# Performance work log

Measured on AMD Instinct MI355X. Metric: run time of the kernel, lower is better.

The kernel has to match this reference:

```python
import jax, jax.numpy as jnp
import numpy as np

C = 512
HEADS = 8
HEAD_DIM = 64
OUT = 2560
NEG = -1.0e12
EPS = 1e-5


def _layernorm(x, g, b):
    mu = jnp.mean(x, axis=-1, keepdims=True)
    var = jnp.mean(jnp.square(x - mu), axis=-1, keepdims=True)
    return (x - mu) * jax.lax.rsqrt(var + EPS) * g + b


def setup_inputs() -> dict:
    key = jax.random.key(0)
    ks = jax.random.split(key, 16)
    s = 0.02
    return {
        "x": jax.random.normal(ks[0], (8, C, 32, 32), dtype=jnp.float32),
        "conv_w": jax.random.normal(ks[1], (C, C), dtype=jnp.float32) * s,
        "conv_b": jnp.zeros((C,), jnp.float32),
        "ln_g": jnp.ones((C,), jnp.float32),
        "ln_b": jnp.zeros((C,), jnp.float32),
        "qkv_w": jax.random.normal(ks[2], (3 * C, C), dtype=jnp.float32) * s,
        "qkv_b": jnp.zeros((3 * C,), jnp.float32),
        "proj_w": jax.random.normal(ks[3], (C, C), dtype=jnp.float32) * s,
        "proj_b": jnp.zeros((C,), jnp.float32),
        "w1": jax.random.normal(ks[4], (C, C), dtype=jnp.float32) * s,
        "b1": jnp.zeros((C,), jnp.float32),
        "w2": jax.random.normal(ks[5], (C, C), dtype=jnp.float32) * s,
        "b2": jnp.zeros((C,), jnp.float32),
        "fc_w": jax.random.normal(ks[6], (OUT, C), dtype=jnp.float32) * s,
        "fc_b": jnp.zeros((OUT,), jnp.float32),
    }


def reference(x, conv_w, conv_b, ln_g, ln_b, qkv_w, qkv_b, proj_w, proj_b,
              w1, b1, w2, b2, fc_w, fc_b):
    B, Cc, H, W = x.shape
    N = H * W
    mk = jax.random.split(jax.random.key(42), 3)

    # Flat1D: conv1x1 == per-pixel linear, then flatten -> [B, N, C]
    t = jnp.einsum('bchw,oc->bhwo', x, conv_w) + conv_b
    t = t.reshape(B, N, Cc)

    # LayerNorm (shared params)
    t = _layernorm(t, ln_g, ln_b)

    # Attention with random additive mask (p=0.5)
    qkv = t @ qkv_w.T + qkv_b  # [B, N, 3C]
    qkv = qkv.reshape(B, N, 3, HEADS, Cc // HEADS)
    q = jnp.transpose(qkv[:, :, 0], (0, 2, 1, 3))  # [B, H, N, D]
    k = jnp.transpose(qkv[:, :, 1], (0, 2, 1, 3))
    v = jnp.transpose(qkv[:, :, 2], (0, 2, 1, 3))
    scale = HEAD_DIM ** (-0.5)
    attn = jnp.einsum('bhnd,bhmd->bhnm', q, k) * scale
    amask = jax.random.bernoulli(mk[0], 0.5, attn.shape)
    attn = attn + amask.astype(attn.dtype) * NEG
    attn = jax.nn.softmax(attn, axis=-1)
    o = jnp.einsum('bhnm,bhmd->bhnd', attn, v)
    o = jnp.transpose(o, (0, 2, 1, 3)).reshape(B, N, Cc)
    t = o @ proj_w.T + proj_b

    # FeedForward with random additive masks
    h = jax.nn.gelu(t @ w1.T + b1, approximate=False)
    m1 = jax.random.bernoulli(mk[1], 0.3, h.shape)
    h = h + m1.astype(h.dtype) * NEG
    t = h @ w2.T + b2
    m2 = jax.random.bernoulli(mk[2], 0.1, t.shape)
    t = t + m2.astype(t.dtype) * NEG

    # LayerNorm (same params), mean over tokens, final fc
    t = _layernorm(t, ln_g, ln_b)
    t = jnp.mean(t, axis=1)  # [B, C]
    return t @ fc_w.T + fc_b
```

## Files before the change

kernel.cpp:

```cpp
#include <hip/hip_runtime.h>
#include <stdint.h>
#include <math.h>

#define NEGV -1.0e12f
#define QSCALE 0.18033688011112042f

typedef __attribute__((ext_vector_type(8))) short bf16x8;
typedef __attribute__((ext_vector_type(4))) float f32x4;
typedef __attribute__((ext_vector_type(8))) ushort u16x8;

#define ROTL1(v, r) ({ uint32_t _d;                                            \
    asm("v_alignbit_b32 %0, %1, %1, %2" : "=v"(_d) : "v"(v), "n"(32 - (r)));   \
    _d; })

#if defined(__has_builtin)
#if __has_builtin(__builtin_amdgcn_exp2f)
#define EXP2(x) __builtin_amdgcn_exp2f(x)
#endif
#endif
#ifndef EXP2
#define EXP2(x) exp2f(x)
#endif

__host__ static void tf2x32_host(uint32_t k0, uint32_t k1, uint32_t c0, uint32_t c1,
                                 uint32_t* o0, uint32_t* o1) {
    uint32_t ks2 = k0 ^ k1 ^ 0x1BD11BDAu;
    uint32_t x0 = c0 + k0, x1 = c1 + k1;
#define TF_RND(r) x0 += x1; x1 = ((x1 << (r)) | (x1 >> (32 - (r)))); x1 ^= x0;
    TF_RND(13) TF_RND(15) TF_RND(26) TF_RND(6)
    x0 += k1;  x1 += ks2 + 1u;
    TF_RND(17) TF_RND(29) TF_RND(16) TF_RND(24)
    x0 += ks2; x1 += k0 + 2u;
    TF_RND(13) TF_RND(15) TF_RND(26) TF_RND(6)
    x0 += k0;  x1 += k1 + 3u;
    TF_RND(17) TF_RND(29) TF_RND(16) TF_RND(24)
    x0 += k1;  x1 += ks2 + 4u;
    TF_RND(13) TF_RND(15) TF_RND(26) TF_RND(6)
    x0 += ks2; x1 += k0 + 5u;
#undef TF_RND
    *o0 = x0; *o1 = x1;
}

__device__ __forceinline__ uint32_t tf_bits(uint32_t k0, uint32_t k1, uint32_t j) {
    const uint32_t ks2 = k0 ^ k1 ^ 0x1BD11BDAu;
    uint32_t x0 = k0, x1 = j + k1;
#define TFR(r) x0 += x1; x1 = ROTL1(x1, r); x1 ^= x0;
    TFR(13) TFR(15) TFR(26) TFR(6)
    x0 += k1;  x1 += ks2 + 1u;
    TFR(17) TFR(29) TFR(16) TFR(24)
    x0 += ks2; x1 += k0 + 2u;
    TFR(13) TFR(15) TFR(26) TFR(6)
    x0 += k0;  x1 += k1 + 3u;
    TFR(17) TFR(29) TFR(16) TFR(24)
    x0 += k1;  x1 += ks2 + 4u;
    TFR(13) TFR(15) TFR(26) TFR(6)
#undef TFR
    return (x0 + ks2) ^ (x1 + (k0 + 5u));
}

__host__ static uint32_t maskT(float p) {
    double t = ceil((double)p * 8388608.0);
    return ((uint32_t)t) << 9;
}

__device__ __forceinline__ ushort f2bf(float x) {
    uint32_t u = __float_as_uint(x);
    u += 0x7fffu + ((u >> 16) & 1u);
    return (ushort)(u >> 16);
}
__device__ __forceinline__ float bf2f(ushort u) {
    return __uint_as_float(((uint32_t)u) << 16);
}

__global__ __launch_bounds__(256) void prep_k(const float* __restrict__ x,
                                              ushort* __restrict__ xt,
                                              const float* __restrict__ s0,
                                              const float* __restrict__ s1,
                                              const float* __restrict__ s2,
                                              const float* __restrict__ s3,
                                              const float* __restrict__ s4,
                                              ushort* __restrict__ wdst)
{
    __shared__ float tile[64][65];
    const int tid = threadIdx.x;
    if (blockIdx.x < 1024) {
        const int id = blockIdx.x;
        const int n0 = (id & 15) * 64, c0 = ((id >> 4) & 7) * 64, b = id >> 7;
        const float* src = x + ((size_t)b * 512 + c0) * 1024 + n0;
#pragma unroll
        for (int i = 0; i < 4; ++i) {
            const int r = (tid >> 4) + i * 16;
            const int col = (tid & 15) * 4;
            float4 v = *(const float4*)(src + (size_t)r * 1024 + col);
            tile[r][col + 0] = v.x; tile[r][col + 1] = v.y;
            tile[r][col + 2] = v.z; tile[r][col + 3] = v.w;
        }
        __syncthreads();
#pragma unroll
        for (int i = 0; i < 2; ++i) {
            const int nl = (tid >> 3) + i * 32;
            const int cb = (tid & 7) * 8;
            u16x8 o;
#pragma unroll
            for (int j = 0; j < 8; ++j) o[j] = f2bf(tile[cb + j][nl]);
            *(u16x8*)(xt + ((size_t)b * 1024 + n0 + nl) * 512 + c0 + cb) = o;
        }
    } else {
        const size_t i = ((size_t)(blockIdx.x - 1024) * 256 + tid) * 8;
        const float* src; size_t off;
        if (i < 262144)       { src = s0; off = 0; }
        else if (i < 1048576) { src = s1; off = 262144; }
        else if (i < 1310720) { src = s2; off = 1048576; }
        else if (i < 1572864) { src = s3; off = 1310720; }
        else                  { src = s4; off = 1572864; }
        const float* p = src + (i - off);
        float4 a = *(const float4*)p;
        float4 b = *(const float4*)(p + 4);
        u16x8 o;
        o[0] = f2bf(a.x); o[1] = f2bf(a.y); o[2] = f2bf(a.z); o[3] = f2bf(a.w);
        o[4] = f2bf(b.x); o[5] = f2bf(b.y); o[6] = f2bf(b.z); o[7] = f2bf(b.w);
        *(u16x8*)(wdst + i) = o;
    }
}

template<int EPI>
__global__ __launch_bounds__(256) void bgemm_k(
    const ushort* __restrict__ A, const ushort* __restrict__ W,
    const float* __restrict__ bias,
    ushort* __restrict__ outb,
    ushort* __restrict__ qb, ushort* __restrict__ kb, ushort* __restrict__ vb)
{
    const int tid = threadIdx.x;
    const int wave = tid >> 6, lane = tid & 63;
    const int lg = lane >> 4, lc = lane & 15;
    const int m0 = blockIdx.x * 128 + wave * 32;
    const int o0 = blockIdx.y * 64;

    f32x4 acc[2][4];
#pragma unroll
    for (int i = 0; i < 2; ++i)
#pragma unroll
        for (int j = 0; j < 4; ++j) acc[i][j] = (f32x4){0.f, 0.f, 0.f, 0.f};

    const ushort* Ab = A + (size_t)(m0 + lc) * 512 + lg * 8;
    const ushort* Wb = W + (size_t)(o0 + lc) * 512 + lg * 8;

#pragma unroll 4
    for (int k0 = 0; k0 < 512; k0 += 32) {
        bf16x8 aq[2], bw[4];
        aq[0] = *(const bf16x8*)(Ab + k0);
        aq[1] = *(const bf16x8*)(Ab + 16 * 512 + k0);
#pragma unroll
        for (int j = 0; j < 4; ++j) bw[j] = *(const bf16x8*)(Wb + (size_t)j * 16 * 512 + k0);
#pragma unroll
        for (int i = 0; i < 2; ++i)
#pragma unroll
            for (int j = 0; j < 4; ++j)
                acc[i][j] = __builtin_amdgcn_mfma_f32_16x16x32_bf16(aq[i], bw[j], acc[i][j], 0, 0, 0);
    }

    float bvv[4];
#pragma unroll
    for (int j = 0; j < 4; ++j) bvv[j] = bias[o0 + j * 16 + lc];

#pragma unroll
    for (int i = 0; i < 2; ++i) {
#pragma unroll
        for (int j = 0; j < 4; ++j) {
#pragma unroll
            for (int r = 0; r < 4; ++r) {
                const int m = m0 + i * 16 + lg * 4 + r;
                const int o = o0 + j * 16 + lc;
                float v = acc[i][j][r] + bvv[j];
                if constexpr (EPI == 4) {
                    outb[(size_t)m * 512 + o] = f2bf(v);
                } else {
                    const int s = o >> 9, hh = (o >> 6) & 7, d = o & 63;
                    const int b = m >> 10, n = m & 1023;
                    const int bh = b * 8 + hh;
                    ushort* dst = (s == 0) ? qb : (s == 1) ? kb : vb;
                    const float scl = (s == 0) ? QSCALE : 1.0f;
                    dst[((size_t)bh * 1024 + n) * 64 + d] = f2bf(v * scl);
                }
            }
        }
    }
}

__global__ __launch_bounds__(256) void vxpose_k(const ushort* __restrict__ v,
                                                ushort* __restrict__ vt)
{
    __shared__ ushort tile[64][72];
    const int tid = threadIdx.x;
    const int bh = blockIdx.y, n0 = blockIdx.x * 64;
    const int row = tid >> 2, cq = (tid & 3) * 16;
    const ushort* src = v + ((size_t)bh * 1024 + n0 + row) * 64 + cq;
    *(u16x8*)&tile[row][cq] = *(const u16x8*)src;
    *(u16x8*)&tile[row][cq + 8] = *(const u16x8*)(src + 8);
    __syncthreads();
    const int d = tid >> 2, nq = (tid & 3) * 16;
    u16x8 o0v, o1v;
#pragma unroll
    for (int i = 0; i < 8; ++i) o0v[i] = tile[nq + i][d];
#pragma unroll
    for (int i = 0; i < 8; ++i) o1v[i] = tile[nq + 8 + i][d];
    ushort* dst = vt + ((size_t)bh * 64 + d) * 1024 + n0 + nq;
    *(u16x8*)dst = o0v;
    *(u16x8*)(dst + 8) = o1v;
}

__global__ __launch_bounds__(256) void ln_k(const ushort* __restrict__ in,
                                            const float* __restrict__ g,
                                            const float* __restrict__ bb,
                                            ushort* __restrict__ outb)
{
    const int wave = threadIdx.x >> 6, lane = threadIdx.x & 63;
    const size_t tok = (size_t)blockIdx.x * 4 + wave;
    const ushort* row = in + tok * 512;
    const int c0 = lane * 8;
    u16x8 vv = *(const u16x8*)(row + c0);
    float x[8];
#pragma unroll
    for (int i = 0; i < 8; i++) x[i] = bf2f(vv[i]);
    float s = 0.f;
#pragma unroll
    for (int i = 0; i < 8; i++) s += x[i];
#pragma unroll
    for (int sh = 32; sh; sh >>= 1) s += __shfl_xor(s, sh, 64);
    const float mu = s * (1.0f / 512.0f);
    float vsum = 0.f;
#pragma unroll
    for (int i = 0; i < 8; i++) { float d = x[i] - mu; vsum += d * d; }
#pragma unroll
    for (int sh = 32; sh; sh >>= 1) vsum += __shfl_xor(vsum, sh, 64);
    const float inv = 1.0f / sqrtf(vsum * (1.0f / 512.0f) + 1e-5f);
    float4 g0 = *(const float4*)(g + c0);
    float4 g1 = *(const float4*)(g + c0 + 4);
    float4 b0 = *(const float4*)(bb + c0);
    float4 b1 = *(const float4*)(bb + c0 + 4);
    float gg[8] = {g0.x, g0.y, g0.z, g0.w, g1.x, g1.y, g1.z, g1.w};
    float bv[8] = {b0.x, b0.y, b0.z, b0.w, b1.x, b1.y, b1.z, b1.w};
    u16x8 o;
#pragma unroll
    for (int i = 0; i < 8; i++) o[i] = f2bf((x[i] - mu) * inv * gg[i] + bv[i]);
    *(u16x8*)(outb + tok * 512 + c0) = o;
}

__global__ __launch_bounds__(512) void mega_k(
    const ushort* __restrict__ qb, const ushort* __restrict__ kb,
    const ushort* __restrict__ vtb,
    const ushort* __restrict__ wproj, const float* __restrict__ pjb,
    const ushort* __restrict__ ww1, const float* __restrict__ b1v,
    const ushort* __restrict__ ww2, const float* __restrict__ b2v,
    const float* __restrict__ g, const float* __restrict__ bln,
    float* __restrict__ pblock,
    uint32_t km0, uint32_t km1, uint32_t k10, uint32_t k11,
    uint32_t k20, uint32_t k21, uint32_t T1, uint32_t T2)
{
    __shared__ ushort bufA[16][520];
    __shared__ ushort plds[8][16][40];
    __shared__ float stats[16][8][2];
    const int tid = threadIdx.x;
    const int wave = tid >> 6, lane = tid & 63;
    const int lg = lane >> 4, lc = lane & 15;
    const int b = blockIdx.x & 7, tg = blockIdx.x >> 3;
    const int bh = b * 8 + wave;
    const int q0 = tg * 16;

    const ushort* qp = qb + (size_t)bh * 65536;
    bf16x8 aq0 = *(const bf16x8*)(qp + (size_t)(q0 + lc) * 64 + lg * 8);
    bf16x8 aq1 = *(const bf16x8*)(qp + (size_t)(q0 + lc) * 64 + 32 + lg * 8);

    f32x4 zero = {0.f, 0.f, 0.f, 0.f};
    f32x4 oacc[4] = {zero, zero, zero, zero};
    float D[4] = {0.f, 0.f, 0.f, 0.f};

    uint32_t jr[4];
#pragma unroll
    for (int r = 0; r < 4; ++r)
        jr[r] = ((uint32_t)bh * 1024u + (uint32_t)(q0 + lg * 4 + r)) * 1024u + (uint32_t)lc;

    const ushort* krow = kb + (size_t)bh * 65536 + (size_t)lc * 64 + lg * 8;
    const ushort* vrow = vtb + (size_t)bh * 65536 + (size_t)lc * 1024 + lg * 8;

    for (int ch = 0; ch < 32; ++ch) {
        bf16x8 bk00 = *(const bf16x8*)(krow);
        bf16x8 bk01 = *(const bf16x8*)(krow + 32);
        bf16x8 bk10 = *(const bf16x8*)(krow + 1024);
        bf16x8 bk11 = *(const bf16x8*)(krow + 1056);

        f32x4 s0 = __builtin_amdgcn_mfma_f32_16x16x32_bf16(aq0, bk00, zero, 0, 0, 0);
        s0 = __builtin_amdgcn_mfma_f32_16x16x32_bf16(aq1, bk01, s0, 0, 0, 0);
        f32x4 s1 = __builtin_amdgcn_mfma_f32_16x16x32_bf16(aq0, bk10, zero, 0, 0, 0);
        s1 = __builtin_amdgcn_mfma_f32_16x16x32_bf16(aq1, bk11, s1, 0, 0, 0);

#pragma unroll
        for (int r = 0; r < 4; ++r) {
            const uint32_t bits0 = tf_bits(km0, km1, jr[r]);
            const uint32_t bits1 = tf_bits(km0, km1, jr[r] + 16u);
            jr[r] += 32u;
            const float pv0 = ((int)bits0 < 0) ? EXP2(s0[r]) : 0.f;
            const float pv1 = ((int)bits1 < 0) ? EXP2(s1[r]) : 0.f;
            D[r] += pv0 + pv1;
            uint32_t pk;
            asm("v_cvt_pk_bf16_f32 %0, %1, %2" : "=v"(pk) : "v"(pv0), "v"(pv1));
            plds[wave][lg * 4 + r][lc] = (ushort)pk;
            plds[wave][lg * 4 + r][lc + 16] = (ushort)(pk >> 16);
        }

        bf16x8 pa = *(const bf16x8*)&plds[wave][lc][lg * 8];

#pragma unroll
        for (int dt = 0; dt < 4; ++dt) {
            bf16x8 bv = *(const bf16x8*)(vrow + (size_t)dt * 16384);
            oacc[dt] = __builtin_amdgcn_mfma_f32_16x16x32_bf16(pa, bv, oacc[dt], 0, 0, 0);
        }
        krow += 2048;
        vrow += 32;
    }

#pragma unroll
    for (int r = 0; r < 4; ++r) {
#pragma unroll
        for (int sh = 1; sh < 16; sh <<= 1) D[r] += __shfl_xor(D[r], sh, 64);
    }

#pragma unroll
    for (int r = 0; r < 4; ++r) {
        const int row = lg * 4 + r;
        const float inv = 1.0f / D[r];
#pragma unroll
        for (int dt = 0; dt < 4; ++dt)
            bufA[row][wave * 64 + dt * 16 + lc] = f2bf(oacc[dt][r] * inv);
    }
    __syncthreads();

    const int o0 = wave * 64;
    const int mg0 = b * 1024 + tg * 16 + lg * 4;

    f32x4 acc[4] = {zero, zero, zero, zero};
    {
        const ushort* Wb = wproj + (size_t)(o0 + lc) * 512 + lg * 8;
#pragma unroll 4
        for (int k0 = 0; k0 < 512; k0 += 32) {
            bf16x8 a0 = *(const bf16x8*)&bufA[lc][k0 + lg * 8];
#pragma unroll
            for (int j = 0; j < 4; ++j) {
                bf16x8 bw = *(const bf16x8*)(Wb + (size_t)j * 16 * 512 + k0);
                acc[j] = __builtin_amdgcn_mfma_f32_16x16x32_bf16(a0, bw, acc[j], 0, 0, 0);
            }
        }
    }
    float bias4[4];
#pragma unroll
    for (int j = 0; j < 4; ++j) bias4[j] = pjb[o0 + j * 16 + lc];
    __syncthreads();
#pragma unroll
    for (int j = 0; j < 4; ++j)
#pragma unroll
        for (int r = 0; r < 4; ++r)
            bufA[lg * 4 + r][o0 + j * 16 + lc] = f2bf(acc[j][r] + bias4[j]);
    __syncthreads();

#pragma unroll
    for (int j = 0; j < 4; ++j) acc[j] = zero;
    {
        const ushort* Wb = ww1 + (size_t)(o0 + lc) * 512 + lg * 8;
#pragma unroll 4
        for (int k0 = 0; k0 < 512; k0 += 32) {
            bf16x8 a0 = *(const bf16x8*)&bufA[lc][k0 + lg * 8];
#pragma unroll
            for (int j = 0; j < 4; ++j) {
                bf16x8 bw = *(const bf16x8*)(Wb + (size_t)j * 16 * 512 + k0);
                acc[j] = __builtin_amdgcn_mfma_f32_16x16x32_bf16(a0, bw, acc[j], 0, 0, 0);
            }
        }
    }
#pragma unroll
    for (int j = 0; j < 4; ++j) bias4[j] = b1v[o0 + j * 16 + lc];
    __syncthreads();
#pragma unroll
    for (int j = 0; j < 4; ++j) {
#pragma unroll
        for (int r = 0; r < 4; ++r) {
            float v = acc[j][r] + bias4[j];
            v = 0.5f * v * (1.0f + erff(v * 0.70710678118654752f));
            const uint32_t jidx = (uint32_t)((mg0 + r) * 512 + o0 + j * 16 + lc);
            if (tf_bits(k10, k11, jidx) < T1) v += NEGV;
            bufA[lg * 4 + r][o0 + j * 16 + lc] = f2bf(v);
        }
    }
    __syncthreads();

#pragma unroll
    for (int j = 0; j < 4; ++j) acc[j] = zero;
    {
        const ushort* Wb = ww2 + (size_t)(o0 + lc) * 512 + lg * 8;
#pragma unroll 4
        for (int k0 = 0; k0 < 512; k0 += 32) {
            bf16x8 a0 = *(const bf16x8*)&bufA[lc][k0 + lg * 8];
#pragma unroll
            for (int j = 0; j < 4; ++j) {
                bf16x8 bw = *(const bf16x8*)(Wb + (size_t)j * 16 * 512 + k0);
                acc[j] = __builtin_amdgcn_mfma_f32_16x16x32_bf16(a0, bw, acc[j], 0, 0, 0);
            }
        }
    }
#pragma unroll
    for (int j = 0; j < 4; ++j) bias4[j] = b2v[o0 + j * 16 + lc];
    float t2v[4][4];
#pragma unroll
    for (int j = 0; j < 4; ++j) {
#pragma unroll
        for (int r = 0; r < 4; ++r) {
            float v = acc[j][r] + bias4[j];
            const uint32_t jidx = (uint32_t)((mg0 + r) * 512 + o0 + j * 16 + lc);
            if (tf_bits(k20, k21, jidx) < T2) v += NEGV;
            t2v[j][r] = v;
        }
    }

    float rs[4], rq[4];
#pragma unroll
    for (int r = 0; r < 4; ++r) {
        float s = 0.f, q = 0.f;
#pragma unroll
        for (int j = 0; j < 4; ++j) { s += t2v[j][r]; q += t2v[j][r] * t2v[j][r]; }
#pragma unroll
        for (int sh = 1; sh < 16; sh <<= 1) {
            s += __shfl_xor(s, sh, 64);
            q += __shfl_xor(q, sh, 64);
        }
        rs[r] = s; rq[r] = q;
    }
    if (lc == 0) {
#pragma unroll
        for (int r = 0; r < 4; ++r) {
            stats[lg * 4 + r][wave][0] = rs[r];
            stats[lg * 4 + r][wave][1] = rq[r];
        }
    }
    __syncthreads();
    float mu[4], inv[4];
#pragma unroll
    for (int r = 0; r < 4; ++r) {
        float S = 0.f, S2 = 0.f;
#pragma unroll
        for (int w = 0; w < 8; ++w) { S += stats[lg * 4 + r][w][0]; S2 += stats[lg * 4 + r][w][1]; }
        const float m = S * (1.0f / 512.0f);
        const float var = S2 * (1.0f / 512.0f) - m * m;
        mu[r] = m;
        inv[r] = 1.0f / sqrtf(var + 1e-5f);
    }
    float gld[4], bld[4];
#pragma unroll
    for (int j = 0; j < 4; ++j) {
        gld[j] = g[o0 + j * 16 + lc];
        bld[j] = bln[o0 + j * 16 + lc];
    }
    float ps[4] = {0.f, 0.f, 0.f, 0.f};
#pragma unroll
    for (int j = 0; j < 4; ++j) {
#pragma unroll
        for (int r = 0; r < 4; ++r)
            ps[j] += (t2v[j][r] - mu[r]) * inv[r] * gld[j] + bld[j];
    }
#pragma unroll
    for (int j = 0; j < 4; ++j) {
        ps[j] += __shfl_xor(ps[j], 16, 64);
        ps[j] += __shfl_xor(ps[j], 32, 64);
    }
    if (lg == 0) {
#pragma unroll
        for (int j = 0; j < 4; ++j)
            pblock[((size_t)(b * 64 + tg)) * 512 + o0 + j * 16 + lc] = ps[j];
    }
}

__global__ __launch_bounds__(256) void mred2_k(const float* __restrict__ pblock,
                                               float* __restrict__ tm)
{
    const int b = blockIdx.y;
    const int c = blockIdx.x * 256 + threadIdx.x;
    const float* p = pblock + (size_t)b * 64 * 512 + c;
    float s = 0.f;
#pragma unroll 8
    for (int t = 0; t < 64; ++t) s += p[(size_t)t * 512];
    tm[b * 512 + c] = s * (1.0f / 1024.0f);
}

__global__ __launch_bounds__(256) void fc_k(const float* __restrict__ tm,
                                            const float* __restrict__ w,
                                            const float* __restrict__ bias,
                                            float* __restrict__ outp)
{
    const int b = blockIdx.y;
    const int o = blockIdx.x * 256 + threadIdx.x;
    const float* tr = tm + b * 512;
    const float* wr = w + (size_t)o * 512;
    float s = 0.f;
    for (int k = 0; k < 512; k += 4) {
        float4 a = *(const float4*)(tr + k);
        float4 ww = *(const float4*)(wr + k);
        s = fmaf(a.x, ww.x, s); s = fmaf(a.y, ww.y, s);
        s = fmaf(a.z, ww.z, s); s = fmaf(a.w, ww.w, s);
    }
    outp[b * 2560 + o] = s + bias[o];
}

extern "C" void kernel_launch(void* const* d_in, const int* in_sizes, int n_in,
                              void* d_out, int out_size, void* d_ws, size_t ws_size,
                              hipStream_t stream)
{
    const float* x      = (const float*)d_in[0];
    const float* conv_w = (const float*)d_in[1];
    const float* conv_b = (const float*)d_in[2];
    const float* ln_g   = (const float*)d_in[3];
    const float* ln_b   = (const float*)d_in[4];
    const float* qkv_w  = (const float*)d_in[5];
    const float* qkv_b  = (const float*)d_in[6];
    const float* proj_w = (const float*)d_in[7];
    const float* proj_b = (const float*)d_in[8];
    const float* w1     = (const float*)d_in[9];
    const float* b1     = (const float*)d_in[10];
    const float* w2     = (const float*)d_in[11];
    const float* b2     = (const float*)d_in[12];
    const float* fc_w   = (const float*)d_in[13];
    const float* fc_b   = (const float*)d_in[14];
    float* out = (float*)d_out;

    if (ws_size < (size_t)71303168) return;

    uint32_t mk0a, mk0b, mk1a, mk1b, mk2a, mk2b;
    tf2x32_host(0u, 42u, 0u, 0u, &mk0a, &mk0b);
    tf2x32_host(0u, 42u, 0u, 1u, &mk1a, &mk1b);
    tf2x32_host(0u, 42u, 0u, 2u, &mk2a, &mk2b);
    const uint32_t T_m1 = maskT(0.3f);
    const uint32_t T_m2 = maskT(0.1f);

    char* wsb = (char*)d_ws;
    ushort* xt     = (ushort*)wsb;
    ushort* wts    = (ushort*)(wsb + 8388608);
    ushort* qbuf   = (ushort*)(wsb + 12582912);
    ushort* kbuf   = (ushort*)(wsb + 20971520);
    ushort* vbuf   = (ushort*)(wsb + 29360128);
    ushort* vtbuf  = (ushort*)(wsb + 37748736);
    ushort* convbf = (ushort*)(wsb + 46137344);
    ushort* ln1bf  = (ushort*)(wsb + 54525952);
    float*  pblock = (float*)(wsb + 62914560);
    float*  tm     = (float*)(wsb + 64487424);

    ushort* wconv = wts;
    ushort* wqkv  = wts + 262144;
    ushort* wproj = wts + 1048576;
    ushort* ww1   = wts + 1310720;
    ushort* ww2   = wts + 1572864;

    dim3 blk(256);
    prep_k<<<dim3(1920), blk, 0, stream>>>(x, xt, conv_w, qkv_w, proj_w, w1, w2, wts);
    bgemm_k<4><<<dim3(64, 8), blk, 0, stream>>>(xt, wconv, conv_b, convbf,
                                                nullptr, nullptr, nullptr);
    ln_k<<<dim3(2048), blk, 0, stream>>>(convbf, ln_g, ln_b, ln1bf);
    bgemm_k<1><<<dim3(64, 24), blk, 0, stream>>>(ln1bf, wqkv, qkv_b, nullptr,
                                                 qbuf, kbuf, vbuf);
    vxpose_k<<<dim3(16, 64), blk, 0, stream>>>(vbuf, vtbuf);
    mega_k<<<dim3(512), dim3(512), 0, stream>>>(qbuf, kbuf, vtbuf,
                                                wproj, proj_b, ww1, b1, ww2, b2,
                                                ln_g, ln_b, pblock,
                                                mk0a, mk0b, mk1a, mk1b, mk2a, mk2b,
                                                T_m1, T_m2);
    mred2_k<<<dim3(2, 8), blk, 0, stream>>>(pblock, tm);
    fc_k<<<dim3(10, 8), blk, 0, stream>>>(tm, fc_w, fc_b, out);
}
```

Baseline: 354.2 us.

## Fuse conv+LayerNorm and QKV+V-transpose, split mega kernel into attention and FFN

The conv GEMM now runs LayerNorm in its epilogue through an LDS tile, and the QKV GEMM writes V already transposed through shared memory. Both changes remove a kernel launch and a full bf16 round trip through global memory. The monolithic attention+FFN kernel is split into an attention kernel with 256 threads and 1024 blocks, which writes O to global, and a separate FFN kernel that reloads it. The split trades an extra O round trip for better parallelism and occupancy in attention. The convln kernel only launches 256 blocks of 32 rows, so it may underfill the device.

```diff
diff --git a/kernel.cpp b/kernel.cpp
--- a/kernel.cpp
+++ b/kernel.cpp
@@ -123,13 +123,103 @@
     }
 }
 
-template<int EPI>
-__global__ __launch_bounds__(256) void bgemm_k(
+__global__ __launch_bounds__(256) void convln_k(
     const ushort* __restrict__ A, const ushort* __restrict__ W,
     const float* __restrict__ bias,
-    ushort* __restrict__ outb,
-    ushort* __restrict__ qb, ushort* __restrict__ kb, ushort* __restrict__ vb)
-{
+    const float* __restrict__ g, const float* __restrict__ bln,
+    ushort* __restrict__ outb)
+{
+    __shared__ ushort cbuf[32][520];
+    const int tid = threadIdx.x;
+    const int wave = tid >> 6, lane = tid & 63;
+    const int lg = lane >> 4, lc = lane & 15;
+    const int m0 = blockIdx.x * 32;
+
+    f32x4 acc[2][2][4];
+#pragma unroll
+    for (int t = 0; t < 2; ++t)
+#pragma unroll
+        for (int i = 0; i < 2; ++i)
+#pragma unroll
+            for (int j = 0; j < 4; ++j) acc[t][i][j] = (f32x4){0.f, 0.f, 0.f, 0.f};
+
+    const ushort* Ab = A + (size_t)(m0 + lc) * 512 + lg * 8;
+    const ushort* Wb0 = W + (size_t)(wave * 64 + lc) * 512 + lg * 8;
+    const ushort* Wb1 = W + (size_t)(256 + wave * 64 + lc) * 512 + lg * 8;
+
+#pragma unroll 4
+    for (int k0 = 0; k0 < 512; k0 += 32) {
+        bf16x8 aq[2], bw0[4], bw1[4];
+        aq[0] = *(const bf16x8*)(Ab + k0);
+        aq[1] = *(const bf16x8*)(Ab + 16 * 512 + k0);
+#pragma unroll
+        for (int j = 0; j < 4; ++j) {
+            bw0[j] = *(const bf16x8*)(Wb0 + (size_t)j * 16 * 512 + k0);
+            bw1[j] = *(const bf16x8*)(Wb1 + (size_t)j * 16 * 512 + k0);
+        }
+#pragma unroll
+        for (int i = 0; i < 2; ++i)
+#pragma unroll
+            for (int j = 0; j < 4; ++j) {
+                acc[0][i][j] = __builtin_amdgcn_mfma_f32_16x16x32_bf16(aq[i], bw0[j], acc[0][i][j], 0, 0, 0);
+                acc[1][i][j] = __builtin_amdgcn_mfma_f32_16x16x32_bf16(aq[i], bw1[j], acc[1][i][j], 0, 0, 0);
+            }
+    }
+
+#pragma unroll
+    for (int t = 0; t < 2; ++t) {
+        const int o0 = t * 256 + wave * 64;
+#pragma unroll
+        for (int j = 0; j < 4; ++j) {
+            const float bv = bias[o0 + j * 16 + lc];
+#pragma unroll
+            for (int i = 0; i < 2; ++i)
+#pragma unroll
+                for (int r = 0; r < 4; ++r)
+                    cbuf[i * 16 + lg * 4 + r][o0 + j * 16 + lc] = f2bf(acc[t][i][j][r] + bv);
+        }
+    }
+    __syncthreads();
+
+    const int c0 = lane * 8;
+    float4 g0 = *(const float4*)(g + c0);
+    float4 g1 = *(const float4*)(g + c0 + 4);
+    float4 b0 = *(const float4*)(bln + c0);
+    float4 b1 = *(const float4*)(bln + c0 + 4);
+    float gg[8] = {g0.x, g0.y, g0.z, g0.w, g1.x, g1.y, g1.z, g1.w};
+    float bv8[8] = {b0.x, b0.y, b0.z, b0.w, b1.x, b1.y, b1.z, b1.w};
+#pragma unroll
+    for (int tt = 0; tt < 8; ++tt) {
+        const int row = wave * 8 + tt;
+        u16x8 vv = *(const u16x8*)&cbuf[row][c0];
+        float xv[8];
+#pragma unroll
+        for (int i = 0; i < 8; i++) xv[i] = bf2f(vv[i]);
+        float s = 0.f;
+#pragma unroll
+        for (int i = 0; i < 8; i++) s += xv[i];
+#pragma unroll
+        for (int sh = 32; sh; sh >>= 1) s += __shfl_xor(s, sh, 64);
+        const float mu = s * (1.0f / 512.0f);
+        float vs = 0.f;
+#pragma unroll
+        for (int i = 0; i < 8; i++) { float d = xv[i] - mu; vs += d * d; }
+#pragma unroll
+        for (int sh = 32; sh; sh >>= 1) vs += __shfl_xor(vs, sh, 64);
+        const float inv = 1.0f / sqrtf(vs * (1.0f / 512.0f) + 1e-5f);
+        u16x8 o;
+#pragma unroll
+        for (int i = 0; i < 8; i++) o[i] = f2bf((xv[i] - mu) * inv * gg[i] + bv8[i]);
+        *(u16x8*)(outb + (size_t)(m0 + row) * 512 + c0) = o;
+    }
+}
+
+__global__ __launch_bounds__(256) void qkvvt_k(
+    const ushort* __restrict__ A, const ushort* __restrict__ W,
+    const float* __restrict__ bias,
+    ushort* __restrict__ qb, ushort* __restrict__ kb, ushort* __restrict__ vtb)
+{
+    __shared__ ushort vtile[64][136];
     const int tid = threadIdx.x;
     const int wave = tid >> 6, lane = tid & 63;
     const int lg = lane >> 4, lc = lane & 15;
@@ -163,111 +253,67 @@
 #pragma unroll
     for (int j = 0; j < 4; ++j) bvv[j] = bias[o0 + j * 16 + lc];
 
-#pragma unroll
-    for (int i = 0; i < 2; ++i) {
-#pragma unroll
-        for (int j = 0; j < 4; ++j) {
-#pragma unroll
-            for (int r = 0; r < 4; ++r) {
-                const int m = m0 + i * 16 + lg * 4 + r;
-                const int o = o0 + j * 16 + lc;
-                float v = acc[i][j][r] + bvv[j];
-                if constexpr (EPI == 4) {
-                    outb[(size_t)m * 512 + o] = f2bf(v);
-                } else {
+    if (blockIdx.y < 16) {
+#pragma unroll
+        for (int i = 0; i < 2; ++i) {
+#pragma unroll
+            for (int j = 0; j < 4; ++j) {
+#pragma unroll
+                for (int r = 0; r < 4; ++r) {
+                    const int m = m0 + i * 16 + lg * 4 + r;
+                    const int o = o0 + j * 16 + lc;
+                    float v = acc[i][j][r] + bvv[j];
                     const int s = o >> 9, hh = (o >> 6) & 7, d = o & 63;
                     const int b = m >> 10, n = m & 1023;
                     const int bh = b * 8 + hh;
-                    ushort* dst = (s == 0) ? qb : (s == 1) ? kb : vb;
+                    ushort* dst = (s == 0) ? qb : kb;
                     const float scl = (s == 0) ? QSCALE : 1.0f;
                     dst[((size_t)bh * 1024 + n) * 64 + d] = f2bf(v * scl);
                 }
             }
         }
-    }
-}
-
-__global__ __launch_bounds__(256) void vxpose_k(const ushort* __restrict__ v,
-                                                ushort* __restrict__ vt)
-{
-    __shared__ ushort tile[64][72];
-    const int tid = threadIdx.x;
-    const int bh = blockIdx.y, n0 = blockIdx.x * 64;
-    const int row = tid >> 2, cq = (tid & 3) * 16;
-    const ushort* src = v + ((size_t)bh * 1024 + n0 + row) * 64 + cq;
-    *(u16x8*)&tile[row][cq] = *(const u16x8*)src;
-    *(u16x8*)&tile[row][cq + 8] = *(const u16x8*)(src + 8);
-    __syncthreads();
-    const int d = tid >> 2, nq = (tid & 3) * 16;
-    u16x8 o0v, o1v;
-#pragma unroll
-    for (int i = 0; i < 8; ++i) o0v[i] = tile[nq + i][d];
-#pragma unroll
-    for (int i = 0; i < 8; ++i) o1v[i] = tile[nq + 8 + i][d];
-    ushort* dst = vt + ((size_t)bh * 64 + d) * 1024 + n0 + nq;
-    *(u16x8*)dst = o0v;
-    *(u16x8*)(dst + 8) = o1v;
-}
-
-__global__ __launch_bounds__(256) void ln_k(const ushort* __restrict__ in,
-                                            const float* __restrict__ g,
-                                            const float* __restrict__ bb,
-                                            ushort* __restrict__ outb)
-{
-    const int wave = threadIdx.x >> 6, lane = threadIdx.x & 63;
-    const size_t tok = (size_t)blockIdx.x * 4 + wave;
-    const ushort* row = in + tok * 512;
-    const int c0 = lane * 8;
-    u16x8 vv = *(const u16x8*)(row + c0);
-    float x[8];
-#pragma unroll
-    for (int i = 0; i < 8; i++) x[i] = bf2f(vv[i]);
-    float s = 0.f;
-#pragma unroll
-    for (int i = 0; i < 8; i++) s += x[i];
-#pragma unroll
-    for (int sh = 32; sh; sh >>= 1) s += __shfl_xor(s, sh, 64);
-    const float mu = s * (1.0f / 512.0f);
-    float vsum = 0.f;
-#pragma unroll
-    for (int i = 0; i < 8; i++) { float d = x[i] - mu; vsum += d * d; }
-#pragma unroll
-    for (int sh = 32; sh; sh >>= 1) vsum += __shfl_xor(vsum, sh, 64);
-    const float inv = 1.0f / sqrtf(vsum * (1.0f / 512.0f) + 1e-5f);
-    float4 g0 = *(const float4*)(g + c0);
-    float4 g1 = *(const float4*)(g + c0 + 4);
-    float4 b0 = *(const float4*)(bb + c0);
-    float4 b1 = *(const float4*)(bb + c0 + 4);
-    float gg[8] = {g0.x, g0.y, g0.z, g0.w, g1.x, g1.y, g1.z, g1.w};
-    float bv[8] = {b0.x, b0.y, b0.z, b0.w, b1.x, b1.y, b1.z, b1.w};
-    u16x8 o;
-#pragma unroll
-    for (int i = 0; i < 8; i++) o[i] = f2bf((x[i] - mu) * inv * gg[i] + bv[i]);
-    *(u16x8*)(outb + tok * 512 + c0) = o;
-}
-
-__global__ __launch_bounds__(512) void mega_k(
+    } else {
+        const int mloc0 = wave * 32;
+#pragma unroll
+        for (int i = 0; i < 2; ++i)
+#pragma unroll
+            for (int j = 0; j < 4; ++j)
+#pragma unroll
+                for (int r = 0; r < 4; ++r)
+                    vtile[j * 16 + lc][mloc0 + i * 16 + lg * 4 + r] = f2bf(acc[i][j][r] + bvv[j]);
+        __syncthreads();
+        const int hh = blockIdx.y - 16;
+        const int mb0 = blockIdx.x * 128;
+        const int b = mb0 >> 10, n0 = mb0 & 1023;
+        const int bh = b * 8 + hh;
+        const int d = tid >> 2, ng = (tid & 3) * 32;
+        ushort* dst = vtb + ((size_t)bh * 64 + d) * 1024 + n0 + ng;
+#pragma unroll
+        for (int q8 = 0; q8 < 4; ++q8) {
+            u16x8 o;
+#pragma unroll
+            for (int e = 0; e < 8; ++e) o[e] = vtile[d][ng + q8 * 8 + e];
+            *(u16x8*)(dst + q8 * 8) = o;
+        }
+    }
+}
+
+__global__ __launch_bounds__(256) void attn_k(
     const ushort* __restrict__ qb, const ushort* __restrict__ kb,
-    const ushort* __restrict__ vtb,
-    const ushort* __restrict__ wproj, const float* __restrict__ pjb,
-    const ushort* __restrict__ ww1, const float* __restrict__ b1v,
-    const ushort* __restrict__ ww2, const float* __restrict__ b2v,
-    const float* __restrict__ g, const float* __restrict__ bln,
-    float* __restrict__ pblock,
-    uint32_t km0, uint32_t km1, uint32_t k10, uint32_t k11,
-    uint32_t k20, uint32_t k21, uint32_t T1, uint32_t T2)
-{
-    __shared__ ushort bufA[16][520];
-    __shared__ ushort plds[8][16][40];
-    __shared__ float stats[16][8][2];
+    const ushort* __restrict__ vtb, ushort* __restrict__ ob,
+    uint32_t km0, uint32_t km1)
+{
+    __shared__ ushort plds[4][16][40];
     const int tid = threadIdx.x;
     const int wave = tid >> 6, lane = tid & 63;
+    const int bh = blockIdx.x & 63;
+    const int qt = blockIdx.x >> 6;
+    const int b = bh >> 3, h = bh & 7;
+    const int q0 = qt * 64 + wave * 16;
     const int lg = lane >> 4, lc = lane & 15;
-    const int b = blockIdx.x & 7, tg = blockIdx.x >> 3;
-    const int bh = b * 8 + wave;
-    const int q0 = tg * 16;
 
     const ushort* qp = qb + (size_t)bh * 65536;
+
     bf16x8 aq0 = *(const bf16x8*)(qp + (size_t)(q0 + lc) * 64 + lg * 8);
     bf16x8 aq1 = *(const bf16x8*)(qp + (size_t)(q0 + lc) * 64 + 32 + lg * 8);
 
@@ -327,16 +373,42 @@
 
 #pragma unroll
     for (int r = 0; r < 4; ++r) {
-        const int row = lg * 4 + r;
+        const int q = q0 + lg * 4 + r;
         const float inv = 1.0f / D[r];
-#pragma unroll
-        for (int dt = 0; dt < 4; ++dt)
-            bufA[row][wave * 64 + dt * 16 + lc] = f2bf(oacc[dt][r] * inv);
+        ushort* orow = ob + ((size_t)b * 1024 + q) * 512 + h * 64;
+#pragma unroll
+        for (int dt = 0; dt < 4; ++dt) orow[dt * 16 + lc] = f2bf(oacc[dt][r] * inv);
+    }
+}
+
+__global__ __launch_bounds__(512) void ff_k(
+    const ushort* __restrict__ ob,
+    const ushort* __restrict__ wproj, const float* __restrict__ pjb,
+    const ushort* __restrict__ ww1, const float* __restrict__ b1v,
+    const ushort* __restrict__ ww2, const float* __restrict__ b2v,
+    const float* __restrict__ g, const float* __restrict__ bln,
+    float* __restrict__ pblock,
+    uint32_t k10, uint32_t k11, uint32_t k20, uint32_t k21,
+    uint32_t T1, uint32_t T2)
+{
+    __shared__ ushort bufA[16][520];
+    __shared__ float stats[16][8][2];
+    const int tid = threadIdx.x;
+    const int wave = tid >> 6, lane = tid & 63;
+    const int lg = lane >> 4, lc = lane & 15;
+    const int b = blockIdx.x & 7, tg = blockIdx.x >> 3;
+
+    {
+        const int row = tid >> 5, c0 = (tid & 31) * 16;
+        const ushort* src = ob + ((size_t)(b * 1024 + tg * 16 + row)) * 512 + c0;
+        *(u16x8*)&bufA[row][c0] = *(const u16x8*)src;
+        *(u16x8*)&bufA[row][c0 + 8] = *(const u16x8*)(src + 8);
     }
     __syncthreads();
 
     const int o0 = wave * 64;
     const int mg0 = b * 1024 + tg * 16 + lg * 4;
+    f32x4 zero = {0.f, 0.f, 0.f, 0.f};
 
     f32x4 acc[4] = {zero, zero, zero, zero};
     {
@@ -529,7 +601,7 @@
     const float* fc_b   = (const float*)d_in[14];
     float* out = (float*)d_out;
 
-    if (ws_size < (size_t)71303168) return;
+    if (ws_size < (size_t)67108864) return;
 
     uint32_t mk0a, mk0b, mk1a, mk1b, mk2a, mk2b;
     tf2x32_host(0u, 42u, 0u, 0u, &mk0a, &mk0b);
@@ -543,12 +615,11 @@
     ushort* wts    = (ushort*)(wsb + 8388608);
     ushort* qbuf   = (ushort*)(wsb + 12582912);
     ushort* kbuf   = (ushort*)(wsb + 20971520);
-    ushort* vbuf   = (ushort*)(wsb + 29360128);
-    ushort* vtbuf  = (ushort*)(wsb + 37748736);
-    ushort* convbf = (ushort*)(wsb + 46137344);
-    ushort* ln1bf  = (ushort*)(wsb + 54525952);
-    float*  pblock = (float*)(wsb + 62914560);
-    float*  tm     = (float*)(wsb + 64487424);
+    ushort* vtbuf  = (ushort*)(wsb + 29360128);
+    ushort* ln1bf  = (ushort*)(wsb + 37748736);
+    float*  pblock = (float*)(wsb + 46137344);
+    float*  tm     = (float*)(wsb + 47710208);
+    ushort* obuf   = xt;
 
     ushort* wconv = wts;
     ushort* wqkv  = wts + 262144;
@@ -558,17 +629,12 @@
 
     dim3 blk(256);
     prep_k<<<dim3(1920), blk, 0, stream>>>(x, xt, conv_w, qkv_w, proj_w, w1, w2, wts);
-    bgemm_k<4><<<dim3(64, 8), blk, 0, stream>>>(xt, wconv, conv_b, convbf,
-                                                nullptr, nullptr, nullptr);
-    ln_k<<<dim3(2048), blk, 0, stream>>>(convbf, ln_g, ln_b, ln1bf);
-    bgemm_k<1><<<dim3(64, 24), blk, 0, stream>>>(ln1bf, wqkv, qkv_b, nullptr,
-                                                 qbuf, kbuf, vbuf);
-    vxpose_k<<<dim3(16, 64), blk, 0, stream>>>(vbuf, vtbuf);
-    mega_k<<<dim3(512), dim3(512), 0, stream>>>(qbuf, kbuf, vtbuf,
-                                                wproj, proj_b, ww1, b1, ww2, b2,
-                                                ln_g, ln_b, pblock,
-                                                mk0a, mk0b, mk1a, mk1b, mk2a, mk2b,
-                                                T_m1, T_m2);
+    convln_k<<<dim3(256), blk, 0, stream>>>(xt, wconv, conv_b, ln_g, ln_b, ln1bf);
+    qkvvt_k<<<dim3(64, 24), blk, 0, stream>>>(ln1bf, wqkv, qkv_b, qbuf, kbuf, vtbuf);
+    attn_k<<<dim3(1024), blk, 0, stream>>>(qbuf, kbuf, vtbuf, obuf, mk0a, mk0b);
+    ff_k<<<dim3(512), dim3(512), 0, stream>>>(obuf, wproj, proj_b, ww1, b1, ww2, b2,
+                                              ln_g, ln_b, pblock,
+                                              mk1a, mk1b, mk2a, mk2b, T_m1, T_m2);
     mred2_k<<<dim3(2, 8), blk, 0, stream>>>(pblock, tm);
     fc_k<<<dim3(10, 8), blk, 0, stream>>>(tm, fc_w, fc_b, out);
 }
```

New measurement: 350.5 us. No clear change (-1.0%).
